# Kernel optimization log

Hardware: AMD Instinct MI355X
Metric: run time of the kernel (lower is better)

The kernel has to match this reference:

```python
import jax, jax.numpy as jnp
import numpy as np

WS = 16          # window_size
HS = 8           # halo_size
NH = 4           # num_heads
DIM = 128
WSH = WS + 2 * HS  # 32, window with halo
B, H, W = 2, 128, 128


def _rel_pos_index():
    # static relative-position index table, (WSH^2, WSH^2), int
    r = np.arange(-HS, WS + HS)
    coords = np.stack(np.meshgrid(r, r, indexing='ij'))        # (2, WSH, WSH)
    cf = coords.reshape(2, -1)                                  # (2, WSH^2)
    rel = (cf[:, :, None] - cf[:, None, :]).transpose(1, 2, 0)  # (L, L, 2)
    rel = rel.copy()
    rel[..., 0] += WS + HS - 1
    rel[..., 1] += WS + HS - 1
    rel[..., 0] *= 2 * WS + 2 * HS - 1
    return rel.sum(-1)  # (1024, 1024)

_RPI = _rel_pos_index()


def setup_inputs() -> dict:
    key = jax.random.key(0)
    ks = jax.random.split(key, 10)
    p = lambda k, shp: (jax.random.normal(k, shp, dtype=jnp.float32) * 0.02)
    return {
        'x': jax.random.normal(ks[0], (B, H, W, DIM), dtype=jnp.float32),
        'Wq': p(ks[1], (DIM, DIM)), 'bq': jnp.zeros((DIM,), jnp.float32),
        'Wk': p(ks[2], (DIM, DIM)), 'bk': jnp.zeros((DIM,), jnp.float32),
        'Wv': p(ks[3], (DIM, DIM)), 'bv': jnp.zeros((DIM,), jnp.float32),
        'Wp': p(ks[4], (DIM, DIM)), 'bp': jnp.zeros((DIM,), jnp.float32),
        'bias_table': p(ks[5], ((2 * WS + 2 * HS - 1) ** 2, NH)),
        'shift_size': 0,
    }


def reference(x, Wq, bq, Wk, bk, Wv, bv, Wp, bp, bias_table, shift_size):
    Bx, Hx, Wx, C = x.shape
    hd = C // NH
    scale = hd ** -0.5
    if shift_size > 0:
        x = jnp.roll(x, (-shift_size, -shift_size), axis=(1, 2))
    # reflect-pad by halo and gather overlapping 32x32 windows (stride 16)
    xp = jnp.pad(x, ((0, 0), (HS, HS), (HS, HS), (0, 0)), mode='reflect')
    nWh, nWw = Hx // WS, Wx // WS
    rows = (jnp.arange(nWh) * WS)[:, None] + jnp.arange(WSH)   # (nWh, 32)
    cols = (jnp.arange(nWw) * WS)[:, None] + jnp.arange(WSH)   # (nWw, 32)
    w = xp[:, rows]                 # (B, nWh, 32, Wp, C)
    w = w[:, :, :, cols]            # (B, nWh, 32, nWw, 32, C)
    w = w.transpose(0, 1, 3, 2, 4, 5).reshape(-1, WSH, WSH, C)  # (B*nW, 32, 32, C)
    center = w[:, HS:HS + WS, HS:HS + WS].reshape(-1, WS * WS, C)   # (nWb, 256, C)
    kv = w.reshape(-1, WSH * WSH, C)                                # (nWb, 1024, C)
    q = (center @ Wq.T + bq).reshape(-1, WS * WS, NH, hd).transpose(0, 2, 1, 3)
    k = (kv @ Wk.T + bk).reshape(-1, WSH * WSH, NH, hd).transpose(0, 2, 1, 3)
    v = (kv @ Wv.T + bv).reshape(-1, WSH * WSH, NH, hd).transpose(0, 2, 1, 3)
    attn = jnp.einsum('bhqd,bhkd->bhqk', q, k) * scale   # (nWb, H, 256, 1024)
    bias = bias_table[_RPI.reshape(-1)].reshape(WSH * WSH, WSH * WSH, NH)
    bias = bias.transpose(2, 0, 1)                        # (H, 1024, 1024)
    start = HS * 2 * WS                                   # 256, as in source
    attn = attn + bias[:, start:start + WS * WS, :][None]
    attn = jax.nn.softmax(attn, axis=-1)
    out = jnp.einsum('bhqk,bhkd->bhqd', attn, v)
    out = out.transpose(0, 2, 1, 3).reshape(-1, WS * WS, C)
    out = out @ Wp.T + bp
    out = out.reshape(Bx, nWh, nWw, WS, WS, C).transpose(0, 1, 3, 2, 4, 5)
    out = out.reshape(Bx, Hx, Wx, C)
    if shift_size > 0:
        out = jnp.roll(out, (shift_size, shift_size), axis=(1, 2))
    return out
```

## Files before the change

kernel.cpp:

```cpp
#include <hip/hip_runtime.h>


typedef unsigned short ushort_t;
typedef __attribute__((ext_vector_type(8))) short bf16x8;
typedef __attribute__((ext_vector_type(4))) float floatx4;

#define NHEADS 4
#define BTBL 2209
#define PK 72
#define QSCALE 0.17677669529663687f

__device__ __forceinline__ int reflect_idx(int p) {
    p = (p < 0) ? -p : p;
    p = (p > 127) ? 254 - p : p;
    return p;
}

__device__ __forceinline__ ushort_t f2b(float x) {
    unsigned u = __float_as_uint(x);
    return (ushort_t)((u + 0x7fffu + ((u >> 16) & 1u)) >> 16);
}

__global__ __launch_bounds__(256) void pack_w(
    const float* __restrict__ Wq, const float* __restrict__ Wk,
    const float* __restrict__ Wv, const float* __restrict__ Wp,
    const float* __restrict__ bq, const float* __restrict__ bk,
    const float* __restrict__ bv, const float* __restrict__ bp,
    ushort_t* __restrict__ Wqkv, ushort_t* __restrict__ Wpb,
    float* __restrict__ bqkv, float* __restrict__ bpb)
{
    int idx = blockIdx.x * 256 + threadIdx.x;
    if (idx < 16384)       Wqkv[idx] = f2b(Wq[idx]);
    else if (idx < 32768)  Wqkv[idx] = f2b(Wk[idx - 16384]);
    else if (idx < 49152)  Wqkv[idx] = f2b(Wv[idx - 32768]);
    else if (idx < 65536)  Wpb[idx - 49152] = f2b(Wp[idx - 49152]);
    else {
        int e = idx - 65536;
        for (int k = e; k < 512; k += 256) {
            if (k < 128)      bqkv[k] = bq[k];
            else if (k < 256) bqkv[k] = bk[k - 128];
            else if (k < 384) bqkv[k] = bv[k - 256];
            else              bpb[k - 384] = bp[k - 384];
        }
    }
}

__global__ __launch_bounds__(256) void bias_frag(
    const float* __restrict__ bt, float* __restrict__ bf)
{
    int idx = blockIdx.x * 256 + threadIdx.x;
    int reg  = idx & 3;
    int lane = (idx >> 2) & 63;
    int qt   = (idx >> 8) & 15;
    int kt   = (idx >> 12) & 63;
    int h    = idx >> 18;
    int key  = kt * 16 + ((lane >> 4) << 2) + reg;
    int q    = qt * 16 + (lane & 15);
    int kr = key >> 5, kc = key & 31;
    int bidx = ((q >> 5) + 31 - kr) * 47 + (q & 31) - kc + 23;
    if (bidx < 0) bidx += BTBL;
    bf[idx] = bt[bidx * NHEADS + h];
}

template <bool IN_BF16, bool OUT_BF16>
__global__ __launch_bounds__(256) void gemm_mfma(
    const void* __restrict__ Xv, const ushort_t* __restrict__ W,
    const float* __restrict__ bias, void* __restrict__ Yv,
    const int ldy, const float scale0)
{
    __shared__ ushort_t Xs[128 * 136];

    const int t    = threadIdx.x;
    const int w    = t >> 6;
    const int lane = t & 63;
    const int quad = lane >> 4;
    const int l15  = lane & 15;
    const int m0   = blockIdx.x * 128;
    const int nb   = blockIdx.y;
    const float sc = (nb == 0) ? scale0 : 1.0f;

    if (IN_BF16) {
        const ushort_t* X = (const ushort_t*)Xv;
        #pragma unroll
        for (int i = 0; i < 8; ++i) {
            int s = t + i * 256;
            int row = s >> 4, c8 = s & 15;
            *(int4*)&Xs[row * 136 + c8 * 8] =
                *(const int4*)&X[(size_t)(m0 + row) * 128 + c8 * 8];
        }
    } else {
        const float* X = (const float*)Xv;
        #pragma unroll
        for (int i = 0; i < 16; ++i) {
            int s = t + i * 256;
            int row = s >> 5, c4 = s & 31;
            float4 v = *(const float4*)&X[(size_t)(m0 + row) * 128 + c4 * 4];
            uint2 pk;
            pk.x = (unsigned)f2b(v.x) | ((unsigned)f2b(v.y) << 16);
            pk.y = (unsigned)f2b(v.z) | ((unsigned)f2b(v.w) << 16);
            *(uint2*)&Xs[row * 136 + c4 * 4] = pk;
        }
    }
    __syncthreads();

    float bv[8];
    #pragma unroll
    for (int nt = 0; nt < 8; ++nt) bv[nt] = bias[nb * 128 + nt * 16 + l15];

    floatx4 acc[2][8];
    #pragma unroll
    for (int mt = 0; mt < 2; ++mt)
        #pragma unroll
        for (int nt = 0; nt < 8; ++nt)
            acc[mt][nt] = (floatx4)(bv[nt]);

    #pragma unroll
    for (int kc = 0; kc < 4; ++kc) {
        bf16x8 af[2], bf[8];
        #pragma unroll
        for (int mt = 0; mt < 2; ++mt)
            af[mt] = *(const bf16x8*)&Xs[(w * 32 + mt * 16 + l15) * 136 + kc * 32 + quad * 8];
        #pragma unroll
        for (int nt = 0; nt < 8; ++nt)
            bf[nt] = *(const bf16x8*)&W[(size_t)(nb * 128 + nt * 16 + l15) * 128 + kc * 32 + quad * 8];
        #pragma unroll
        for (int mt = 0; mt < 2; ++mt)
            #pragma unroll
            for (int nt = 0; nt < 8; ++nt)
                acc[mt][nt] = __builtin_amdgcn_mfma_f32_16x16x32_bf16(af[mt], bf[nt], acc[mt][nt], 0, 0, 0);
    }

    #pragma unroll
    for (int mt = 0; mt < 2; ++mt) {
        #pragma unroll
        for (int r = 0; r < 4; ++r) {
            int m = m0 + w * 32 + mt * 16 + quad * 4 + r;
            #pragma unroll
            for (int nt = 0; nt < 8; ++nt) {
                int n = nb * 128 + nt * 16 + l15;
                float y = acc[mt][nt][r] * sc;
                if (OUT_BF16)
                    ((ushort_t*)Yv)[(size_t)m * ldy + n] = f2b(y);
                else
                    ((float*)Yv)[(size_t)m * ldy + n] = y;
            }
        }
    }
}

__global__ __launch_bounds__(256, 2) void halo_attn(
    const ushort_t* __restrict__ QKV,
    const float*    __restrict__ biasf,
    ushort_t* __restrict__ O)
{
    __shared__ ushort_t P_lds[4 * 64 * PK];
    __shared__ ushort_t Vt_lds[4 * 32 * PK];

    const int t    = threadIdx.x;
    const int wave = t >> 6;
    const int lane = t & 63;
    const int quad = lane >> 4;
    const int l15  = lane & 15;

    const int win  = blockIdx.x;
    const int head = blockIdx.y;
    const int b    = win >> 6;
    const int wh   = (win >> 3) & 7;
    const int ww   = win & 7;

    bf16x8 qf[4];
    int qpix[4];
    #pragma unroll
    for (int qt = 0; qt < 4; ++qt) {
        int q_abs = wave * 64 + qt * 16 + l15;
        int gy = wh * 16 + (q_abs >> 4), gx = ww * 16 + (q_abs & 15);
        int pix = (b * 128 + gy) * 128 + gx;
        qpix[qt] = pix;
        qf[qt] = *(const bf16x8*)(QKV + (size_t)pix * 384 + head * 32 + quad * 8);
    }

    floatx4 Oa[2][4];
    #pragma unroll
    for (int dt = 0; dt < 2; ++dt)
        #pragma unroll
        for (int qt = 0; qt < 4; ++qt)
            Oa[dt][qt] = (floatx4)0.f;
    float l[4] = {0.f, 0.f, 0.f, 0.f};

    ushort_t* Pw  = P_lds  + wave * 64 * PK;
    ushort_t* Vtw = Vt_lds + wave * 32 * PK;

    for (int c = 0; c < 16; ++c) {
        {
            int keyv = c * 64 + lane;
            int ky = reflect_idx(wh * 16 + (keyv >> 5) - 8);
            int kx = reflect_idx(ww * 16 + (keyv & 31) - 8);
            int pixv = (b * 128 + ky) * 128 + kx;
            const int4* vp4 = (const int4*)(QKV + (size_t)pixv * 384 + 256 + head * 32);
            int4 vw0 = vp4[0], vw1 = vp4[1], vw2 = vp4[2], vw3 = vp4[3];
            const ushort_t* vs0 = (const ushort_t*)&vw0;
            const ushort_t* vs1 = (const ushort_t*)&vw1;
            const ushort_t* vs2 = (const ushort_t*)&vw2;
            const ushort_t* vs3 = (const ushort_t*)&vw3;
            #pragma unroll
            for (int d = 0; d < 8; ++d) {
                Vtw[(d +  0) * PK + lane] = vs0[d];
                Vtw[(d +  8) * PK + lane] = vs1[d];
                Vtw[(d + 16) * PK + lane] = vs2[d];
                Vtw[(d + 24) * PK + lane] = vs3[d];
            }
        }

        bf16x8 kf[4];
        #pragma unroll
        for (int kt = 0; kt < 4; ++kt) {
            int key = c * 64 + kt * 16 + l15;
            int ky = reflect_idx(wh * 16 + (key >> 5) - 8);
            int kx = reflect_idx(ww * 16 + (key & 31) - 8);
            int pixk = (b * 128 + ky) * 128 + kx;
            kf[kt] = *(const bf16x8*)(QKV + (size_t)pixk * 384 + 128 + head * 32 + quad * 8);
        }

        floatx4 S[4][4];
        #pragma unroll
        for (int kt = 0; kt < 4; ++kt) {
            int kt_abs = c * 4 + kt;
            #pragma unroll
            for (int qt = 0; qt < 4; ++qt) {
                size_t off = ((((size_t)head * 64 + kt_abs) * 16 + (wave * 4 + qt)) * 64 + lane) * 4;
                S[kt][qt] = *(const floatx4*)(biasf + off);
            }
        }
        #pragma unroll
        for (int kt = 0; kt < 4; ++kt)
            #pragma unroll
            for (int qt = 0; qt < 4; ++qt)
                S[kt][qt] = __builtin_amdgcn_mfma_f32_16x16x32_bf16(kf[kt], qf[qt], S[kt][qt], 0, 0, 0);

        #pragma unroll
        for (int qt = 0; qt < 4; ++qt) {
            float ls = 0.f;
            #pragma unroll
            for (int kt = 0; kt < 4; ++kt) {
                #pragma unroll
                for (int r = 0; r < 4; ++r) {
                    float p = __expf(S[kt][qt][r]);
                    S[kt][qt][r] = p;
                    ls += p;
                }
            }
            l[qt] += ls;
            #pragma unroll
            for (int kt = 0; kt < 4; ++kt) {
                uint2 pk;
                pk.x = __builtin_amdgcn_perm(__float_as_uint(S[kt][qt][1]),
                                             __float_as_uint(S[kt][qt][0]), 0x07060302u);
                pk.y = __builtin_amdgcn_perm(__float_as_uint(S[kt][qt][3]),
                                             __float_as_uint(S[kt][qt][2]), 0x07060302u);
                *(uint2*)&Pw[(qt * 16 + l15) * PK + kt * 16 + quad * 4] = pk;
            }
        }

        #pragma unroll
        for (int ks = 0; ks < 2; ++ks) {
            bf16x8 vf[2];
            #pragma unroll
            for (int dt = 0; dt < 2; ++dt)
                vf[dt] = *(const bf16x8*)&Vtw[(dt * 16 + l15) * PK + ks * 32 + quad * 8];
            #pragma unroll
            for (int qt = 0; qt < 4; ++qt) {
                bf16x8 pf = *(const bf16x8*)&Pw[(qt * 16 + l15) * PK + ks * 32 + quad * 8];
                #pragma unroll
                for (int dt = 0; dt < 2; ++dt)
                    Oa[dt][qt] = __builtin_amdgcn_mfma_f32_16x16x32_bf16(vf[dt], pf, Oa[dt][qt], 0, 0, 0);
            }
        }
    }

    #pragma unroll
    for (int qt = 0; qt < 4; ++qt) {
        float lq = l[qt];
        lq += __shfl_xor(lq, 16);
        lq += __shfl_xor(lq, 32);
        float inv = 1.0f / lq;
        #pragma unroll
        for (int dt = 0; dt < 2; ++dt) {
            uint2 pk;
            pk.x = (unsigned)f2b(Oa[dt][qt][0] * inv) | ((unsigned)f2b(Oa[dt][qt][1] * inv) << 16);
            pk.y = (unsigned)f2b(Oa[dt][qt][2] * inv) | ((unsigned)f2b(Oa[dt][qt][3] * inv) << 16);
            *(uint2*)(O + (size_t)qpix[qt] * 128 + head * 32 + dt * 16 + quad * 4) = pk;
        }
    }
}

extern "C" void kernel_launch(void* const* d_in, const int* in_sizes, int n_in,
                              void* d_out, int out_size, void* d_ws, size_t ws_size,
                              hipStream_t stream)
{
    const float* x          = (const float*)d_in[0];
    const float* Wq         = (const float*)d_in[1];
    const float* bq         = (const float*)d_in[2];
    const float* Wk         = (const float*)d_in[3];
    const float* bk         = (const float*)d_in[4];
    const float* Wv         = (const float*)d_in[5];
    const float* bv         = (const float*)d_in[6];
    const float* Wp         = (const float*)d_in[7];
    const float* bp         = (const float*)d_in[8];
    const float* bias_table = (const float*)d_in[9];
    float* out = (float*)d_out;

    const int M = 2 * 128 * 128;
    char* ws = (char*)d_ws;
    ushort_t* Wqkv = (ushort_t*)(ws);
    ushort_t* Wpb  = (ushort_t*)(ws + 98304);
    float*    bqkv = (float*)   (ws + 131072);
    float*    bpb  = (float*)   (ws + 132608);
    ushort_t* QKV  = (ushort_t*)(ws + 133120);
    ushort_t* Ob   = (ushort_t*)(ws + 25298944);
    float*    bf   = (float*)   (ws + 33687552);

    pack_w<<<dim3(257), dim3(256), 0, stream>>>(Wq, Wk, Wv, Wp, bq, bk, bv, bp,
                                                Wqkv, Wpb, bqkv, bpb);
    bias_frag<<<dim3(16384), dim3(256), 0, stream>>>(bias_table, bf);
    gemm_mfma<false, true><<<dim3(256, 3), dim3(256), 0, stream>>>(
        x, Wqkv, bqkv, QKV, 384, QSCALE);
    halo_attn<<<dim3(128, NHEADS), dim3(256), 0, stream>>>(QKV, bf, Ob);
    gemm_mfma<true, false><<<dim3(256, 1), dim3(256), 0, stream>>>(
        Ob, Wpb, bpb, out, 128, 1.0f);
}
```

Measured before the change: 173.4 us.

## Split attention keys across wave halves, store bias as bf16, use exp2

The attention kernel now runs 512 threads per block. Two groups of four waves each process half of the key chunks, and their partial outputs and row sums are combined through LDS at the end. V is staged cooperatively into a shared transposed buffer behind block barriers. The precomputed bias fragment table is stored in bf16 with log2e folded in, and the Q scale also includes log2e so the kernel can use exp2 instead of exp. This halves bias traffic at some precision cost. The QKV GEMM loops over all three output blocks inside one block so the x tile is converted to bf16 once, and the projection GEMM becomes its own specialised kernel.

```diff
diff --git a/kernel.cpp b/kernel.cpp
--- a/kernel.cpp
+++ b/kernel.cpp
@@ -7,8 +7,16 @@
 
 #define NHEADS 4
 #define BTBL 2209
-#define PK 72
-#define QSCALE 0.17677669529663687f
+#define PK 40
+#define VK 72
+#define QS_LOG2E 0.2550348635f
+#define LOG2E 1.4426950408889634f
+
+#if __has_builtin(__builtin_amdgcn_exp2f)
+#define EXP2F(x) __builtin_amdgcn_exp2f(x)
+#else
+#define EXP2F(x) __expf((x) * 0.6931471805599453f)
+#endif
 
 __device__ __forceinline__ int reflect_idx(int p) {
     p = (p < 0) ? -p : p;
@@ -16,9 +24,9 @@
     return p;
 }
 
-__device__ __forceinline__ ushort_t f2b(float x) {
+__device__ __forceinline__ unsigned f2b(float x) {
     unsigned u = __float_as_uint(x);
-    return (ushort_t)((u + 0x7fffu + ((u >> 16) & 1u)) >> 16);
+    return (u + 0x7fffu + ((u >> 16) & 1u)) >> 16;
 }
 
 __global__ __launch_bounds__(256) void pack_w(
@@ -30,10 +38,10 @@
     float* __restrict__ bqkv, float* __restrict__ bpb)
 {
     int idx = blockIdx.x * 256 + threadIdx.x;
-    if (idx < 16384)       Wqkv[idx] = f2b(Wq[idx]);
-    else if (idx < 32768)  Wqkv[idx] = f2b(Wk[idx - 16384]);
-    else if (idx < 49152)  Wqkv[idx] = f2b(Wv[idx - 32768]);
-    else if (idx < 65536)  Wpb[idx - 49152] = f2b(Wp[idx - 49152]);
+    if (idx < 16384)       Wqkv[idx] = (ushort_t)f2b(Wq[idx]);
+    else if (idx < 32768)  Wqkv[idx] = (ushort_t)f2b(Wk[idx - 16384]);
+    else if (idx < 49152)  Wqkv[idx] = (ushort_t)f2b(Wv[idx - 32768]);
+    else if (idx < 65536)  Wpb[idx - 49152] = (ushort_t)f2b(Wp[idx - 49152]);
     else {
         int e = idx - 65536;
         for (int k = e; k < 512; k += 256) {
@@ -46,7 +54,7 @@
 }
 
 __global__ __launch_bounds__(256) void bias_frag(
-    const float* __restrict__ bt, float* __restrict__ bf)
+    const float* __restrict__ bt, ushort_t* __restrict__ bf)
 {
     int idx = blockIdx.x * 256 + threadIdx.x;
     int reg  = idx & 3;
@@ -59,14 +67,12 @@
     int kr = key >> 5, kc = key & 31;
     int bidx = ((q >> 5) + 31 - kr) * 47 + (q & 31) - kc + 23;
     if (bidx < 0) bidx += BTBL;
-    bf[idx] = bt[bidx * NHEADS + h];
-}
-
-template <bool IN_BF16, bool OUT_BF16>
-__global__ __launch_bounds__(256) void gemm_mfma(
-    const void* __restrict__ Xv, const ushort_t* __restrict__ W,
-    const float* __restrict__ bias, void* __restrict__ Yv,
-    const int ldy, const float scale0)
+    bf[idx] = (ushort_t)f2b(bt[bidx * NHEADS + h] * LOG2E);
+}
+
+__global__ __launch_bounds__(256) void gemm_qkv(
+    const float* __restrict__ X, const ushort_t* __restrict__ W,
+    const float* __restrict__ bias, ushort_t* __restrict__ Y)
 {
     __shared__ ushort_t Xs[128 * 136];
 
@@ -76,91 +82,127 @@
     const int quad = lane >> 4;
     const int l15  = lane & 15;
     const int m0   = blockIdx.x * 128;
-    const int nb   = blockIdx.y;
-    const float sc = (nb == 0) ? scale0 : 1.0f;
-
-    if (IN_BF16) {
-        const ushort_t* X = (const ushort_t*)Xv;
-        #pragma unroll
-        for (int i = 0; i < 8; ++i) {
-            int s = t + i * 256;
-            int row = s >> 4, c8 = s & 15;
-            *(int4*)&Xs[row * 136 + c8 * 8] =
-                *(const int4*)&X[(size_t)(m0 + row) * 128 + c8 * 8];
-        }
-    } else {
-        const float* X = (const float*)Xv;
-        #pragma unroll
-        for (int i = 0; i < 16; ++i) {
-            int s = t + i * 256;
-            int row = s >> 5, c4 = s & 31;
-            float4 v = *(const float4*)&X[(size_t)(m0 + row) * 128 + c4 * 4];
-            uint2 pk;
-            pk.x = (unsigned)f2b(v.x) | ((unsigned)f2b(v.y) << 16);
-            pk.y = (unsigned)f2b(v.z) | ((unsigned)f2b(v.w) << 16);
-            *(uint2*)&Xs[row * 136 + c4 * 4] = pk;
-        }
+
+    #pragma unroll
+    for (int i = 0; i < 16; ++i) {
+        int s = t + i * 256;
+        int row = s >> 5, c4 = s & 31;
+        float4 v = *(const float4*)&X[(size_t)(m0 + row) * 128 + c4 * 4];
+        uint2 pk;
+        pk.x = f2b(v.x) | (f2b(v.y) << 16);
+        pk.y = f2b(v.z) | (f2b(v.w) << 16);
+        *(uint2*)&Xs[row * 136 + c4 * 4] = pk;
     }
     __syncthreads();
 
-    float bv[8];
-    #pragma unroll
-    for (int nt = 0; nt < 8; ++nt) bv[nt] = bias[nb * 128 + nt * 16 + l15];
-
-    floatx4 acc[2][8];
-    #pragma unroll
-    for (int mt = 0; mt < 2; ++mt)
-        #pragma unroll
-        for (int nt = 0; nt < 8; ++nt)
-            acc[mt][nt] = (floatx4)(bv[nt]);
-
-    #pragma unroll
-    for (int kc = 0; kc < 4; ++kc) {
-        bf16x8 af[2], bf[8];
-        #pragma unroll
-        for (int mt = 0; mt < 2; ++mt)
-            af[mt] = *(const bf16x8*)&Xs[(w * 32 + mt * 16 + l15) * 136 + kc * 32 + quad * 8];
-        #pragma unroll
-        for (int nt = 0; nt < 8; ++nt)
-            bf[nt] = *(const bf16x8*)&W[(size_t)(nb * 128 + nt * 16 + l15) * 128 + kc * 32 + quad * 8];
-        #pragma unroll
-        for (int mt = 0; mt < 2; ++mt)
+    for (int nb = 0; nb < 3; ++nb) {
+        const float sc = (nb == 0) ? QS_LOG2E : 1.0f;
+        floatx4 acc[2][8];
+        #pragma unroll
+        for (int nt = 0; nt < 8; ++nt) {
+            float bb = bias[nb * 128 + nt * 16 + l15];
+            acc[0][nt] = (floatx4)bb;
+            acc[1][nt] = (floatx4)bb;
+        }
+        #pragma unroll
+        for (int kc = 0; kc < 4; ++kc) {
+            bf16x8 af[2], bfr[8];
+            #pragma unroll
+            for (int mt = 0; mt < 2; ++mt)
+                af[mt] = *(const bf16x8*)&Xs[(w * 32 + mt * 16 + l15) * 136 + kc * 32 + quad * 8];
             #pragma unroll
             for (int nt = 0; nt < 8; ++nt)
-                acc[mt][nt] = __builtin_amdgcn_mfma_f32_16x16x32_bf16(af[mt], bf[nt], acc[mt][nt], 0, 0, 0);
-    }
-
-    #pragma unroll
-    for (int mt = 0; mt < 2; ++mt) {
-        #pragma unroll
-        for (int r = 0; r < 4; ++r) {
-            int m = m0 + w * 32 + mt * 16 + quad * 4 + r;
-            #pragma unroll
-            for (int nt = 0; nt < 8; ++nt) {
-                int n = nb * 128 + nt * 16 + l15;
-                float y = acc[mt][nt][r] * sc;
-                if (OUT_BF16)
-                    ((ushort_t*)Yv)[(size_t)m * ldy + n] = f2b(y);
-                else
-                    ((float*)Yv)[(size_t)m * ldy + n] = y;
+                bfr[nt] = *(const bf16x8*)&W[(size_t)(nb * 128 + nt * 16 + l15) * 128 + kc * 32 + quad * 8];
+            #pragma unroll
+            for (int mt = 0; mt < 2; ++mt)
+                #pragma unroll
+                for (int nt = 0; nt < 8; ++nt)
+                    acc[mt][nt] = __builtin_amdgcn_mfma_f32_16x16x32_bf16(af[mt], bfr[nt], acc[mt][nt], 0, 0, 0);
+        }
+        #pragma unroll
+        for (int mt = 0; mt < 2; ++mt) {
+            #pragma unroll
+            for (int r = 0; r < 4; ++r) {
+                int m = m0 + w * 32 + mt * 16 + quad * 4 + r;
+                #pragma unroll
+                for (int nt = 0; nt < 8; ++nt) {
+                    int n = nb * 128 + nt * 16 + l15;
+                    Y[(size_t)m * 384 + n] = (ushort_t)f2b(acc[mt][nt][r] * sc);
+                }
             }
         }
     }
 }
 
-__global__ __launch_bounds__(256, 2) void halo_attn(
-    const ushort_t* __restrict__ QKV,
-    const float*    __restrict__ biasf,
-    ushort_t* __restrict__ O)
-{
-    __shared__ ushort_t P_lds[4 * 64 * PK];
-    __shared__ ushort_t Vt_lds[4 * 32 * PK];
+__global__ __launch_bounds__(256) void gemm_proj(
+    const ushort_t* __restrict__ X, const ushort_t* __restrict__ W,
+    const float* __restrict__ bias, float* __restrict__ Y)
+{
+    __shared__ ushort_t Xs[128 * 136];
 
     const int t    = threadIdx.x;
-    const int wave = t >> 6;
+    const int w    = t >> 6;
     const int lane = t & 63;
     const int quad = lane >> 4;
     const int l15  = lane & 15;
+    const int m0   = blockIdx.x * 128;
+
+    #pragma unroll
+    for (int i = 0; i < 8; ++i) {
+        int s = t + i * 256;
+        int row = s >> 4, c8 = s & 15;
+        *(int4*)&Xs[row * 136 + c8 * 8] = *(const int4*)&X[(size_t)(m0 + row) * 128 + c8 * 8];
+    }
+    __syncthreads();
+
+    floatx4 acc[2][8];
+    #pragma unroll
+    for (int nt = 0; nt < 8; ++nt) {
+        float bb = bias[nt * 16 + l15];
+        acc[0][nt] = (floatx4)bb;
+        acc[1][nt] = (floatx4)bb;
+    }
+    #pragma unroll
+    for (int kc = 0; kc < 4; ++kc) {
+        bf16x8 af[2], bfr[8];
+        #pragma unroll
+        for (int mt = 0; mt < 2; ++mt)
+            af[mt] = *(const bf16x8*)&Xs[(w * 32 + mt * 16 + l15) * 136 + kc * 32 + quad * 8];
+        #pragma unroll
+        for (int nt = 0; nt < 8; ++nt)
+            bfr[nt] = *(const bf16x8*)&W[(size_t)(nt * 16 + l15) * 128 + kc * 32 + quad * 8];
+        #pragma unroll
+        for (int mt = 0; mt < 2; ++mt)
+            #pragma unroll
+            for (int nt = 0; nt < 8; ++nt)
+                acc[mt][nt] = __builtin_amdgcn_mfma_f32_16x16x32_bf16(af[mt], bfr[nt], acc[mt][nt], 0, 0, 0);
+    }
+    #pragma unroll
+    for (int mt = 0; mt < 2; ++mt)
+        #pragma unroll
+        for (int r = 0; r < 4; ++r) {
+            int m = m0 + w * 32 + mt * 16 + quad * 4 + r;
+            #pragma unroll
+            for (int nt = 0; nt < 8; ++nt)
+                Y[(size_t)m * 128 + nt * 16 + l15] = acc[mt][nt][r];
+        }
+}
+
+__global__ __launch_bounds__(512, 4) void halo_attn(
+    const ushort_t* __restrict__ QKV,
+    const ushort_t* __restrict__ biasf,
+    ushort_t* __restrict__ O)
+{
+    __shared__ ushort_t P_lds[8 * 64 * PK];
+    __shared__ ushort_t Vt_lds[2 * 32 * VK];
+
+    const int t     = threadIdx.x;
+    const int wave  = t >> 6;
+    const int khalf = wave >> 2;
+    const int wq    = wave & 3;
+    const int lane  = t & 63;
+    const int quad  = lane >> 4;
+    const int l15   = lane & 15;
 
     const int win  = blockIdx.x;
     const int head = blockIdx.y;
@@ -172,7 +214,7 @@
     int qpix[4];
     #pragma unroll
     for (int qt = 0; qt < 4; ++qt) {
-        int q_abs = wave * 64 + qt * 16 + l15;
+        int q_abs = wq * 64 + qt * 16 + l15;
         int gy = wh * 16 + (q_abs >> 4), gx = ww * 16 + (q_abs & 15);
         int pix = (b * 128 + gy) * 128 + gx;
         qpix[qt] = pix;
@@ -187,34 +229,31 @@
             Oa[dt][qt] = (floatx4)0.f;
     float l[4] = {0.f, 0.f, 0.f, 0.f};
 
-    ushort_t* Pw  = P_lds  + wave * 64 * PK;
-    ushort_t* Vtw = Vt_lds + wave * 32 * PK;
-
-    for (int c = 0; c < 16; ++c) {
+    ushort_t* Pw  = P_lds + wave * 64 * PK;
+    ushort_t* Vtw = Vt_lds + khalf * 32 * VK;
+
+    for (int c = 0; c < 8; ++c) {
+        const int kc_abs = khalf * 8 + c;
+
+        __syncthreads();
         {
-            int keyv = c * 64 + lane;
-            int ky = reflect_idx(wh * 16 + (keyv >> 5) - 8);
-            int kx = reflect_idx(ww * 16 + (keyv & 31) - 8);
+            int key_local = wq * 16 + l15;
+            int key = kc_abs * 64 + key_local;
+            int ky = reflect_idx(wh * 16 + (key >> 5) - 8);
+            int kx = reflect_idx(ww * 16 + (key & 31) - 8);
             int pixv = (b * 128 + ky) * 128 + kx;
-            const int4* vp4 = (const int4*)(QKV + (size_t)pixv * 384 + 256 + head * 32);
-            int4 vw0 = vp4[0], vw1 = vp4[1], vw2 = vp4[2], vw3 = vp4[3];
-            const ushort_t* vs0 = (const ushort_t*)&vw0;
-            const ushort_t* vs1 = (const ushort_t*)&vw1;
-            const ushort_t* vs2 = (const ushort_t*)&vw2;
-            const ushort_t* vs3 = (const ushort_t*)&vw3;
-            #pragma unroll
-            for (int d = 0; d < 8; ++d) {
-                Vtw[(d +  0) * PK + lane] = vs0[d];
-                Vtw[(d +  8) * PK + lane] = vs1[d];
-                Vtw[(d + 16) * PK + lane] = vs2[d];
-                Vtw[(d + 24) * PK + lane] = vs3[d];
-            }
-        }
+            int4 vv = *(const int4*)(QKV + (size_t)pixv * 384 + 256 + head * 32 + quad * 8);
+            const ushort_t* vs = (const ushort_t*)&vv;
+            #pragma unroll
+            for (int i = 0; i < 8; ++i)
+                Vtw[(quad * 8 + i) * VK + key_local] = vs[i];
+        }
+        __syncthreads();
 
         bf16x8 kf[4];
         #pragma unroll
         for (int kt = 0; kt < 4; ++kt) {
-            int key = c * 64 + kt * 16 + l15;
+            int key = kc_abs * 64 + kt * 16 + l15;
             int ky = reflect_idx(wh * 16 + (key >> 5) - 8);
             int kx = reflect_idx(ww * 16 + (key & 31) - 8);
             int pixk = (b * 128 + ky) * 128 + kx;
@@ -224,11 +263,16 @@
         floatx4 S[4][4];
         #pragma unroll
         for (int kt = 0; kt < 4; ++kt) {
-            int kt_abs = c * 4 + kt;
+            int kt_abs = kc_abs * 4 + kt;
             #pragma unroll
             for (int qt = 0; qt < 4; ++qt) {
-                size_t off = ((((size_t)head * 64 + kt_abs) * 16 + (wave * 4 + qt)) * 64 + lane) * 4;
-                S[kt][qt] = *(const floatx4*)(biasf + off);
+                int qt_abs = wq * 4 + qt;
+                uint2 pk = *(const uint2*)(biasf +
+                    ((((size_t)head * 64 + kt_abs) * 16 + qt_abs) * 64 + lane) * 4);
+                S[kt][qt][0] = __uint_as_float(pk.x << 16);
+                S[kt][qt][1] = __uint_as_float(pk.x & 0xffff0000u);
+                S[kt][qt][2] = __uint_as_float(pk.y << 16);
+                S[kt][qt][3] = __uint_as_float(pk.y & 0xffff0000u);
             }
         }
         #pragma unroll
@@ -241,35 +285,37 @@
         for (int qt = 0; qt < 4; ++qt) {
             float ls = 0.f;
             #pragma unroll
-            for (int kt = 0; kt < 4; ++kt) {
+            for (int kt = 0; kt < 4; ++kt)
                 #pragma unroll
                 for (int r = 0; r < 4; ++r) {
-                    float p = __expf(S[kt][qt][r]);
+                    float p = EXP2F(S[kt][qt][r]);
                     S[kt][qt][r] = p;
                     ls += p;
                 }
-            }
             l[qt] += ls;
-            #pragma unroll
-            for (int kt = 0; kt < 4; ++kt) {
-                uint2 pk;
-                pk.x = __builtin_amdgcn_perm(__float_as_uint(S[kt][qt][1]),
-                                             __float_as_uint(S[kt][qt][0]), 0x07060302u);
-                pk.y = __builtin_amdgcn_perm(__float_as_uint(S[kt][qt][3]),
-                                             __float_as_uint(S[kt][qt][2]), 0x07060302u);
-                *(uint2*)&Pw[(qt * 16 + l15) * PK + kt * 16 + quad * 4] = pk;
-            }
         }
 
         #pragma unroll
         for (int ks = 0; ks < 2; ++ks) {
+            #pragma unroll
+            for (int qt = 0; qt < 4; ++qt)
+                #pragma unroll
+                for (int kh = 0; kh < 2; ++kh) {
+                    int kt = ks * 2 + kh;
+                    uint2 pk;
+                    pk.x = __builtin_amdgcn_perm(__float_as_uint(S[kt][qt][1]),
+                                                 __float_as_uint(S[kt][qt][0]), 0x07060302u);
+                    pk.y = __builtin_amdgcn_perm(__float_as_uint(S[kt][qt][3]),
+                                                 __float_as_uint(S[kt][qt][2]), 0x07060302u);
+                    *(uint2*)&Pw[(qt * 16 + l15) * PK + kh * 16 + quad * 4] = pk;
+                }
             bf16x8 vf[2];
             #pragma unroll
             for (int dt = 0; dt < 2; ++dt)
-                vf[dt] = *(const bf16x8*)&Vtw[(dt * 16 + l15) * PK + ks * 32 + quad * 8];
+                vf[dt] = *(const bf16x8*)&Vtw[(dt * 16 + l15) * VK + ks * 32 + quad * 8];
             #pragma unroll
             for (int qt = 0; qt < 4; ++qt) {
-                bf16x8 pf = *(const bf16x8*)&Pw[(qt * 16 + l15) * PK + ks * 32 + quad * 8];
+                bf16x8 pf = *(const bf16x8*)&Pw[(qt * 16 + l15) * PK + quad * 8];
                 #pragma unroll
                 for (int dt = 0; dt < 2; ++dt)
                     Oa[dt][qt] = __builtin_amdgcn_mfma_f32_16x16x32_bf16(vf[dt], pf, Oa[dt][qt], 0, 0, 0);
@@ -277,18 +323,38 @@
         }
     }
 
-    #pragma unroll
-    for (int qt = 0; qt < 4; ++qt) {
-        float lq = l[qt];
-        lq += __shfl_xor(lq, 16);
-        lq += __shfl_xor(lq, 32);
-        float inv = 1.0f / lq;
-        #pragma unroll
-        for (int dt = 0; dt < 2; ++dt) {
-            uint2 pk;
-            pk.x = (unsigned)f2b(Oa[dt][qt][0] * inv) | ((unsigned)f2b(Oa[dt][qt][1] * inv) << 16);
-            pk.y = (unsigned)f2b(Oa[dt][qt][2] * inv) | ((unsigned)f2b(Oa[dt][qt][3] * inv) << 16);
-            *(uint2*)(O + (size_t)qpix[qt] * 128 + head * 32 + dt * 16 + quad * 4) = pk;
+    __syncthreads();
+    float* slot = (float*)P_lds + (size_t)(wq * 64 + lane) * 40;
+    if (khalf == 1) {
+        #pragma unroll
+        for (int dt = 0; dt < 2; ++dt)
+            #pragma unroll
+            for (int qt = 0; qt < 4; ++qt)
+                *(floatx4*)(slot + (dt * 4 + qt) * 4) = Oa[dt][qt];
+        floatx4 lv = {l[0], l[1], l[2], l[3]};
+        *(floatx4*)(slot + 32) = lv;
+    }
+    __syncthreads();
+    if (khalf == 0) {
+        #pragma unroll
+        for (int dt = 0; dt < 2; ++dt)
+            #pragma unroll
+            for (int qt = 0; qt < 4; ++qt)
+                Oa[dt][qt] += *(const floatx4*)(slot + (dt * 4 + qt) * 4);
+        floatx4 lv = *(const floatx4*)(slot + 32);
+        #pragma unroll
+        for (int qt = 0; qt < 4; ++qt) {
+            float lq = l[qt] + lv[qt];
+            lq += __shfl_xor(lq, 16);
+            lq += __shfl_xor(lq, 32);
+            float inv = 1.0f / lq;
+            #pragma unroll
+            for (int dt = 0; dt < 2; ++dt) {
+                uint2 pk;
+                pk.x = f2b(Oa[dt][qt][0] * inv) | (f2b(Oa[dt][qt][1] * inv) << 16);
+                pk.y = f2b(Oa[dt][qt][2] * inv) | (f2b(Oa[dt][qt][3] * inv) << 16);
+                *(uint2*)(O + (size_t)qpix[qt] * 128 + head * 32 + dt * 16 + quad * 4) = pk;
+            }
         }
     }
 }
@@ -311,20 +377,18 @@
 
     const int M = 2 * 128 * 128;
     char* ws = (char*)d_ws;
-    ushort_t* Wqkv = (ushort_t*)(ws);
-    ushort_t* Wpb  = (ushort_t*)(ws + 98304);
-    float*    bqkv = (float*)   (ws + 131072);
-    float*    bpb  = (float*)   (ws + 132608);
-    ushort_t* QKV  = (ushort_t*)(ws + 133120);
-    ushort_t* Ob   = (ushort_t*)(ws + 25298944);
-    float*    bf   = (float*)   (ws + 33687552);
+    ushort_t* Wqkv  = (ushort_t*)(ws);
+    ushort_t* Wpb   = (ushort_t*)(ws + 98304);
+    float*    bqkv  = (float*)   (ws + 131072);
+    float*    bpb   = (float*)   (ws + 132608);
+    ushort_t* QKV   = (ushort_t*)(ws + 133120);
+    ushort_t* Ob    = (ushort_t*)(ws + 25298944);
+    ushort_t* biasf = (ushort_t*)(ws + 33687552);
 
     pack_w<<<dim3(257), dim3(256), 0, stream>>>(Wq, Wk, Wv, Wp, bq, bk, bv, bp,
                                                 Wqkv, Wpb, bqkv, bpb);
-    bias_frag<<<dim3(16384), dim3(256), 0, stream>>>(bias_table, bf);
-    gemm_mfma<false, true><<<dim3(256, 3), dim3(256), 0, stream>>>(
-        x, Wqkv, bqkv, QKV, 384, QSCALE);
-    halo_attn<<<dim3(128, NHEADS), dim3(256), 0, stream>>>(QKV, bf, Ob);
-    gemm_mfma<true, false><<<dim3(256, 1), dim3(256), 0, stream>>>(
-        Ob, Wpb, bpb, out, 128, 1.0f);
-}
+    bias_frag<<<dim3(16384), dim3(256), 0, stream>>>(bias_table, biasf);
+    gemm_qkv<<<dim3(256), dim3(256), 0, stream>>>(x, Wqkv, bqkv, QKV);
+    halo_attn<<<dim3(128, NHEADS), dim3(512), 0, stream>>>(QKV, biasf, Ob);
+    gemm_proj<<<dim3(256), dim3(256), 0, stream>>>(Ob, Wpb, bpb, out);
+}
```

Measured after the change: 231.6 us. +33.6%, slower.
